# Performance work log

Hardware: AMD Instinct MI355X
Metric: run time of the kernel (lower is better)

## Reference

```python
import jax, jax.numpy as jnp
import numpy as np


def lstm_encode(x, Wih, Whh, b):
    """x: [S, T, F] -> final hidden state [S, H]. PyTorch LSTM gate order (i, f, g, o)."""
    S = x.shape[0]
    H = Whh.shape[1]

    def step(carry, xt):
        h, c = carry
        z = xt @ Wih.T + h @ Whh.T + b  # [S, 4H]
        i, f, g, o = jnp.split(z, 4, axis=-1)
        c = jax.nn.sigmoid(f) * c + jax.nn.sigmoid(i) * jnp.tanh(g)
        h = jax.nn.sigmoid(o) * jnp.tanh(c)
        return (h, c), None

    init = (jnp.zeros((S, H), x.dtype), jnp.zeros((S, H), x.dtype))
    (h, _), _ = jax.lax.scan(step, init, jnp.swapaxes(x, 0, 1))
    return h


def gatv2(h, Ws, Wd, a, bias):
    """Dense GATv2 on batched fully-connected graphs (no self loops).
    h: [G, N, Hin]; Ws, Wd: [nh, Hin, O]; a: [nh, O]; bias: [nh, O] -> [G, N, nh, O].
    Graph is fully connected (all i != j), so edge-softmax == dense row softmax
    with the diagonal masked out; this is the efficient dense form of the
    gather / LeakyReLU / edge-softmax / scatter pattern in DGL's GATv2Conv."""
    nh = Ws.shape[0]
    N = h.shape[1]
    self_mask = jnp.eye(N, dtype=bool)
    outs = []
    for hd in range(nh):  # small fixed head count; loop caps peak memory
        fs = h @ Ws[hd]  # [G, N, O] source-projected feats (messages)
        fd = h @ Wd[hd]  # [G, N, O] dst-projected feats
        e = jax.nn.leaky_relu(fd[:, :, None, :] + fs[:, None, :, :], 0.2)  # [G, dst, src, O]
        logits = jnp.where(self_mask, -jnp.inf, e @ a[hd])  # [G, dst, src]
        attn = jax.nn.softmax(logits, axis=-1)
        outs.append(jnp.einsum('gds,gso->gdo', attn, fs) + bias[hd])
    return jnp.stack(outs, axis=2)


def cosine(x, y, eps=1e-6):
    xn = x / jnp.maximum(jnp.linalg.norm(x, axis=-1, keepdims=True), eps)
    yn = y / jnp.maximum(jnp.linalg.norm(y, axis=-1, keepdims=True), eps)
    return (xn * yn).sum(-1)


def setup_inputs() -> dict:
    key = jax.random.key(0)
    B, K, T, N, F, H, GH, NH = 16, 4, 64, 128, 16, 32, 32, 8
    ks = jax.random.split(key, 16)

    def rn(k, shape, scale=1.0):
        return jax.random.normal(k, shape, jnp.float32) * scale

    return {
        'anchor': rn(ks[0], (B, T, N, F)),
        'pos': rn(ks[1], (B, T, N, F)),
        'neg': rn(ks[2], (B, K, T, N, F)),
        'hideout': rn(ks[3], (B, 2)),
        'timestep': jax.random.uniform(ks[4], (B, 1), jnp.float32),
        'Wih': rn(ks[5], (4 * H, F), 1.0 / np.sqrt(F)),
        'Whh': rn(ks[6], (4 * H, H), 1.0 / np.sqrt(H)),
        'b_lstm': rn(ks[7], (4 * H,), 0.1),
        'W1s': rn(ks[8], (NH, H, H), 1.0 / np.sqrt(H)),
        'W1d': rn(ks[9], (NH, H, H), 1.0 / np.sqrt(H)),
        'a1': rn(ks[10], (NH, H), 1.0 / np.sqrt(H)),
        'b1': rn(ks[11], (NH, H), 0.1),
        'W2s': rn(ks[12], (1, H, GH), 1.0 / np.sqrt(H)),
        'W2d': rn(ks[13], (1, H, GH), 1.0 / np.sqrt(H)),
        'a2': rn(ks[14], (1, GH), 1.0 / np.sqrt(GH)),
        'b2': rn(ks[15], (1, GH), 0.1),
        'num_agents': 128,
    }


def reference(anchor, pos, neg, hideout, timestep, Wih, Whh, b_lstm,
              W1s, W1d, a1, b1, W2s, W2d, a2, b2, num_agents):
    B, T, N, F = anchor.shape
    K = neg.shape[1]
    H = Whh.shape[1]
    # per-agent time series -> LSTM sequences
    a_seq = jnp.transpose(anchor, (0, 2, 1, 3)).reshape(B * N, T, F)
    p_seq = jnp.transpose(pos, (0, 2, 1, 3)).reshape(B * N, T, F)
    n_seq = jnp.transpose(neg, (0, 1, 3, 2, 4)).reshape(B * K * N, T, F)
    hn = lstm_encode(jnp.concatenate([a_seq, p_seq, n_seq], 0), Wih, Whh, b_lstm)
    hg = hn.reshape(-1, N, H)  # [(2+K)*B, N, H] batched fully-connected graphs
    h1 = gatv2(hg, W1s, W1d, a1, b1).mean(axis=2)  # mean over 8 heads
    h2 = gatv2(h1, W2s, W2d, a2, b2)[:, :, 0, :]   # single head, squeezed
    pooled = h2.mean(axis=1)                        # AvgPooling over nodes
    anchor_res = pooled[:B]
    pos_res = pooled[B:2 * B]
    neg_res = pooled[2 * B:].reshape(B, K, -1)
    sim_pos = cosine(anchor_res, pos_res)[:, None]      # [B, 1]
    sim_neg = cosine(anchor_res[:, None, :], neg_res)   # [B, K]
    all_vecs = jnp.concatenate([sim_neg, sim_pos], axis=1)  # positive last
    contrastive = (-jax.nn.log_softmax(all_vecs, axis=1)[:, -1]).mean()
    res = jnp.concatenate([anchor_res, hideout, timestep], axis=-1)
    return res, contrastive
```

## Files before the change

### kernel.cpp

```cpp
#include <hip/hip_runtime.h>
#include <math.h>


typedef __bf16 bf16x8 __attribute__((ext_vector_type(8)));
typedef float  f32x4  __attribute__((ext_vector_type(4)));
typedef unsigned int u32x4 __attribute__((ext_vector_type(4)));

__device__ __forceinline__ float fast_rcp(float x) { return __builtin_amdgcn_rcpf(x); }
__device__ __forceinline__ float sigm(float x)     { return fast_rcp(1.f + __expf(-x)); }
__device__ __forceinline__ float tanh_fast(float x){ return fmaf(2.f, fast_rcp(1.f + __expf(-2.f * x)), -1.f); }

#define KEEP4(x) asm volatile("" : "+v"(x))

#define PAIR_BARRIER() do {                                     \
    asm volatile("s_waitcnt lgkmcnt(0)" ::: "memory");          \
    __builtin_amdgcn_sched_barrier(0);                          \
    __builtin_amdgcn_s_barrier();                               \
    __builtin_amdgcn_sched_barrier(0);                          \
} while (0)

__global__ __launch_bounds__(128, 1) void lstm_mfma_kernel(
    const float* __restrict__ anchor, const float* __restrict__ pos,
    const float* __restrict__ neg, const float* __restrict__ Wih,
    const float* __restrict__ Whh, const float* __restrict__ bias,
    float* __restrict__ hn)
{
    __shared__ unsigned int Hbuf[2][512];
    const int tid  = threadIdx.x;
    const int wid  = tid >> 6;
    const int lane = tid & 63;
    const int l15  = lane & 15;
    const int g4   = lane >> 4;

    #pragma unroll
    for (int i = 0; i < 8; ++i) ((unsigned int*)Hbuf)[tid + i * 128] = 0u;

    u32x4 whhH[4], whhL[4], wihH[4];
    float bq[4];
    #pragma unroll
    for (int G = 0; G < 4; ++G) {
        const int c = G * 32 + wid * 16 + l15;
        bq[G] = bias[c];
        union { u32x4 u; bf16x8 v; } th, tl, ti;
        const float* wr = Whh + c * 32 + g4 * 8;
        #pragma unroll
        for (int i = 0; i < 8; ++i) {
            float wv = wr[i];
            __bf16 hi = (__bf16)wv;
            th.v[i] = hi;
            tl.v[i] = (__bf16)(wv - (float)hi);
        }
        if (g4 < 2) {
            const float* wr2 = Wih + c * 16 + g4 * 8;
            #pragma unroll
            for (int i = 0; i < 8; ++i) ti.v[i] = (__bf16)wr2[i];
        } else {
            #pragma unroll
            for (int i = 0; i < 8; ++i) ti.v[i] = (__bf16)0.f;
        }
        whhH[G] = th.u; whhL[G] = tl.u; wihH[G] = ti.u;
    }
    #pragma unroll
    for (int G = 0; G < 4; ++G) { KEEP4(whhH[G]); KEEP4(whhL[G]); KEEP4(wihH[G]); }

    const int s = blockIdx.x * 16 + l15;
    const float* xbase; int sl;
    if (s < 2048)      { xbase = anchor; sl = s; }
    else if (s < 4096) { xbase = pos;    sl = s - 2048; }
    else               { xbase = neg;    sl = s - 4096; }
    const bool xact = (g4 < 2);
    const float* xp = xbase + (sl >> 7) * 131072 + (sl & 127) * 16 + (xact ? g4 * 8 : 0);

    const float4 z4 = make_float4(0.f, 0.f, 0.f, 0.f);
    float4 xaA = z4, xbA = z4, xaB = z4, xbB = z4;
    if (xact) {
        xaA = *(const float4*)(xp);        xbA = *(const float4*)(xp + 4);
        xaB = *(const float4*)(xp + 2048); xbB = *(const float4*)(xp + 2052);
    }

    float cst[4] = {0,0,0,0};
    float hv[4]  = {0,0,0,0};

    const int c0  = g4 * 2;
    const int swz = (l15 & 3) << 1;
    const int ro0 = l15 * 32 + ((c0 ^ swz) << 2);
    const int ro1 = l15 * 32 + (((c0 + 1) ^ swz) << 2);
    const int jw  = wid * 16 + l15;
    int cur = 0;
    PAIR_BARRIER();

    #define LSTM_STEP(XA, XB)                                                          \
    {                                                                                  \
        const unsigned int* rb = Hbuf[cur];                                            \
        unsigned int*       wb = Hbuf[cur ^ 1];                                        \
        bf16x8 ax;                                                                     \
        ax[0]=(__bf16)XA.x; ax[1]=(__bf16)XA.y; ax[2]=(__bf16)XA.z; ax[3]=(__bf16)XA.w;\
        ax[4]=(__bf16)XB.x; ax[5]=(__bf16)XB.y; ax[6]=(__bf16)XB.z; ax[7]=(__bf16)XB.w;\
        uint4 v0 = *(const uint4*)(rb + ro0);                                          \
        uint4 v1 = *(const uint4*)(rb + ro1);                                          \
        union { unsigned int u[4]; bf16x8 v; } ahi;                                    \
        ahi.u[0] = __builtin_amdgcn_perm(v0.y, v0.x, 0x05040100u);                     \
        ahi.u[1] = __builtin_amdgcn_perm(v0.w, v0.z, 0x05040100u);                     \
        ahi.u[2] = __builtin_amdgcn_perm(v1.y, v1.x, 0x05040100u);                     \
        ahi.u[3] = __builtin_amdgcn_perm(v1.w, v1.z, 0x05040100u);                     \
        f32x4 z[4];                                                                    \
        _Pragma("unroll")                                                              \
        for (int G = 0; G < 4; ++G) {                                                  \
            f32x4 a = __builtin_amdgcn_mfma_f32_16x16x32_bf16(                         \
                ax, __builtin_bit_cast(bf16x8, wihH[G]), (f32x4)(0.f), 0, 0, 0);       \
            a = __builtin_amdgcn_mfma_f32_16x16x32_bf16(                               \
                ahi.v, __builtin_bit_cast(bf16x8, whhH[G]), a, 0, 0, 0);               \
            a = __builtin_amdgcn_mfma_f32_16x16x32_bf16(                               \
                ahi.v, __builtin_bit_cast(bf16x8, whhL[G]), a, 0, 0, 0);               \
            z[G] = a;                                                                  \
        }                                                                              \
        _Pragma("unroll")                                                              \
        for (int r = 0; r < 4; ++r) {                                                  \
            float zi = z[0][r] + bq[0];                                                \
            float zf = z[1][r] + bq[1];                                                \
            float zg = z[2][r] + bq[2];                                                \
            float zo = z[3][r] + bq[3];                                                \
            float cn = fmaf(sigm(zf), cst[r], sigm(zi) * tanh_fast(zg));               \
            cst[r] = cn;                                                               \
            float h = sigm(zo) * tanh_fast(cn);                                        \
            hv[r] = h;                                                                 \
            unsigned int pk = (unsigned int)__builtin_bit_cast(unsigned short,         \
                                                               (__bf16)h);            \
            const int mm = g4 * 4 + r;                                                 \
            wb[mm * 32 + (((jw >> 2) ^ ((mm & 3) << 1)) << 2) + (jw & 3)] = pk;        \
        }                                                                              \
        PAIR_BARRIER();                                                                \
        cur ^= 1;                                                                      \
    }

    for (int t = 0; t < 64; t += 2) {
        float4 cA1 = xaA, cA2 = xbA;
        if (xact && t + 2 < 64) {
            const float* p = xp + (t + 2) * 2048;
            xaA = *(const float4*)(p); xbA = *(const float4*)(p + 4);
        }
        LSTM_STEP(cA1, cA2);

        float4 cB1 = xaB, cB2 = xbB;
        if (xact && t + 3 < 64) {
            const float* p = xp + (t + 3) * 2048;
            xaB = *(const float4*)(p); xbB = *(const float4*)(p + 4);
        }
        LSTM_STEP(cB1, cB2);
    }
    #undef LSTM_STEP

    const int seq0 = blockIdx.x * 16;
    #pragma unroll
    for (int r = 0; r < 4; ++r) {
        hn[(seq0 + g4 * 4 + r) * 32 + jw] = hv[r];
    }
}

__device__ __forceinline__ int fsoff(int n) { return n * 36 + ((n >> 5) << 2); }

__global__ __launch_bounds__(256, 2) void gat1_kernel(
    const float* __restrict__ hn, const float* __restrict__ W1s,
    const float* __restrict__ W1d, const float* __restrict__ a1,
    const float* __restrict__ b1, float* __restrict__ h1heads)
{
    const int g = blockIdx.x >> 3, hd = blockIdx.x & 7;
    __shared__ float FSf[128 * 36 + 16];
    __shared__ float FD[128][36];
    __shared__ float AVr[32];
    __shared__ float As06[128];
    __shared__ float Ad06[128];
    const int tid = threadIdx.x;

    if (tid < 32) AVr[tid] = a1[hd * 32 + tid];

    {
        const int o = tid & 31, nb = tid >> 5;
        float wcs[32], wcd[32];
        const float* wsp = W1s + hd * 1024 + o;
        const float* wdp = W1d + hd * 1024 + o;
        #pragma unroll
        for (int k = 0; k < 32; ++k) { wcs[k] = wsp[k * 32]; wcd[k] = wdp[k * 32]; }
        const float* hp = hn + g * 4096 + nb * 512;
        #pragma unroll 1
        for (int n = 0; n < 16; ++n) {
            const int row = nb * 16 + n;
            float a0 = 0.f, a1_ = 0.f, b0 = 0.f, b1_ = 0.f;
            #pragma unroll
            for (int k0 = 0; k0 < 32; k0 += 4) {
                float4 hv = *(const float4*)(hp + n * 32 + k0);
                a0 = fmaf(hv.x, wcs[k0+0], a0); b0 = fmaf(hv.x, wcd[k0+0], b0);
                a1_ = fmaf(hv.y, wcs[k0+1], a1_); b1_ = fmaf(hv.y, wcd[k0+1], b1_);
                a0 = fmaf(hv.z, wcs[k0+2], a0); b0 = fmaf(hv.z, wcd[k0+2], b0);
                a1_ = fmaf(hv.w, wcs[k0+3], a1_); b1_ = fmaf(hv.w, wcd[k0+3], b1_);
            }
            FSf[fsoff(row) + o] = a0 + a1_;
            FD[row][o] = b0 + b1_;
        }
    }
    __syncthreads();

    if (tid < 128) {
        float ss = 0.f, sd = 0.f;
        const float* fr = FSf + fsoff(tid);
        #pragma unroll
        for (int oo = 0; oo < 32; ++oo) {
            int o = (oo + tid) & 31;
            float a = AVr[o];
            ss = fmaf(a, fr[o], ss);
            sd = fmaf(a, FD[tid][o], sd);
        }
        As06[tid] = 0.6f * ss;
        Ad06[tid] = 0.6f * sd;
    }
    __syncthreads();

    const int p = tid >> 2, sq = tid & 3, sbase = sq << 5;
    const int d0 = p, d1 = p + 64;
    float fdr0[32], fdr1[32], avs[32];
    #pragma unroll
    for (int c = 0; c < 8; ++c) {
        float4 v0 = *(const float4*)&FD[d0][c * 4];
        fdr0[c*4+0] = v0.x; fdr0[c*4+1] = v0.y; fdr0[c*4+2] = v0.z; fdr0[c*4+3] = v0.w;
        float4 v1 = *(const float4*)&FD[d1][c * 4];
        fdr1[c*4+0] = v1.x; fdr1[c*4+1] = v1.y; fdr1[c*4+2] = v1.z; fdr1[c*4+3] = v1.w;
        float4 wv = *(const float4*)&AVr[c * 4];
        avs[c*4+0] = 0.4f * wv.x; avs[c*4+1] = 0.4f * wv.y;
        avs[c*4+2] = 0.4f * wv.z; avs[c*4+3] = 0.4f * wv.w;
    }
    const float adc0 = Ad06[d0], adc1 = Ad06[d1];

    float Z0 = 0.f, Z1 = 0.f;
    float acc0[32], acc1[32];
    #pragma unroll
    for (int o = 0; o < 32; ++o) { acc0[o] = 0.f; acc1[o] = 0.f; }
    #pragma unroll 1
    for (int si = 0; si < 32; ++si) {
        const int s = sbase + si;
        const float* fr = FSf + fsoff(s);
        float4 fa[8];
        #pragma unroll
        for (int c = 0; c < 8; ++c) fa[c] = *(const float4*)(fr + c * 4);
        float c00 = 0.f, c01 = 0.f, c02 = 0.f, c03 = 0.f;
        float c10 = 0.f, c11 = 0.f, c12 = 0.f, c13 = 0.f;
        #pragma unroll
        for (int c = 0; c < 8; ++c) {
            float e;
            e = fdr0[c*4+0] + fa[c].x; c00 = fmaf(avs[c*4+0], __builtin_fabsf(e), c00);
            e = fdr1[c*4+0] + fa[c].x; c10 = fmaf(avs[c*4+0], __builtin_fabsf(e), c10);
            e = fdr0[c*4+1] + fa[c].y; c01 = fmaf(avs[c*4+1], __builtin_fabsf(e), c01);
            e = fdr1[c*4+1] + fa[c].y; c11 = fmaf(avs[c*4+1], __builtin_fabsf(e), c11);
            e = fdr0[c*4+2] + fa[c].z; c02 = fmaf(avs[c*4+2], __builtin_fabsf(e), c02);
            e = fdr1[c*4+2] + fa[c].z; c12 = fmaf(avs[c*4+2], __builtin_fabsf(e), c12);
            e = fdr0[c*4+3] + fa[c].w; c03 = fmaf(avs[c*4+3], __builtin_fabsf(e), c03);
            e = fdr1[c*4+3] + fa[c].w; c13 = fmaf(avs[c*4+3], __builtin_fabsf(e), c13);
        }
        const float ass = As06[s];
        float v0 = adc0 + ass + ((c00 + c01) + (c02 + c03));
        float v1 = adc1 + ass + ((c10 + c11) + (c12 + c13));
        float e0 = (s == d0) ? 0.f : __expf(v0);
        float e1 = (s == d1) ? 0.f : __expf(v1);
        Z0 += e0; Z1 += e1;
        #pragma unroll
        for (int c = 0; c < 8; ++c) {
            acc0[c*4+0] = fmaf(e0, fa[c].x, acc0[c*4+0]);
            acc1[c*4+0] = fmaf(e1, fa[c].x, acc1[c*4+0]);
            acc0[c*4+1] = fmaf(e0, fa[c].y, acc0[c*4+1]);
            acc1[c*4+1] = fmaf(e1, fa[c].y, acc1[c*4+1]);
            acc0[c*4+2] = fmaf(e0, fa[c].z, acc0[c*4+2]);
            acc1[c*4+2] = fmaf(e1, fa[c].z, acc1[c*4+2]);
            acc0[c*4+3] = fmaf(e0, fa[c].w, acc0[c*4+3]);
            acc1[c*4+3] = fmaf(e1, fa[c].w, acc1[c*4+3]);
        }
    }
    Z0 += __shfl_xor(Z0, 1); Z0 += __shfl_xor(Z0, 2);
    Z1 += __shfl_xor(Z1, 1); Z1 += __shfl_xor(Z1, 2);
    const float rz0 = fast_rcp(Z0), rz1 = fast_rcp(Z1);
    #pragma unroll
    for (int o = 0; o < 32; ++o) {
        acc0[o] += __shfl_xor(acc0[o], 1);
        acc0[o] += __shfl_xor(acc0[o], 2);
        acc1[o] += __shfl_xor(acc1[o], 1);
        acc1[o] += __shfl_xor(acc1[o], 2);
    }

    if (sq == 0) {
        const float* bp = b1 + hd * 32;
        float* dst0 = h1heads + ((size_t)((g * 8 + hd) * 128 + d0)) * 32;
        float* dst1 = h1heads + ((size_t)((g * 8 + hd) * 128 + d1)) * 32;
        #pragma unroll
        for (int c = 0; c < 8; ++c) {
            float4 v;
            v.x = fmaf(acc0[c*4+0], rz0, bp[c*4+0]);
            v.y = fmaf(acc0[c*4+1], rz0, bp[c*4+1]);
            v.z = fmaf(acc0[c*4+2], rz0, bp[c*4+2]);
            v.w = fmaf(acc0[c*4+3], rz0, bp[c*4+3]);
            *(float4*)(dst0 + c * 4) = v;
            v.x = fmaf(acc1[c*4+0], rz1, bp[c*4+0]);
            v.y = fmaf(acc1[c*4+1], rz1, bp[c*4+1]);
            v.z = fmaf(acc1[c*4+2], rz1, bp[c*4+2]);
            v.w = fmaf(acc1[c*4+3], rz1, bp[c*4+3]);
            *(float4*)(dst1 + c * 4) = v;
        }
    }
}

__global__ __launch_bounds__(256) void gat2_kernel(
    const float* __restrict__ h1heads, const float* __restrict__ W2s,
    const float* __restrict__ W2d, const float* __restrict__ a2,
    const float* __restrict__ b2, float* __restrict__ pooled)
{
    const int g = blockIdx.x;
    __shared__ float HS[128][36];
    __shared__ float FSf[128 * 36 + 16];
    __shared__ float FD[128][36];
    __shared__ float AVr[32];
    __shared__ float As06[128];
    __shared__ float Ad06[128];
    const int tid = threadIdx.x;

    if (tid < 32) AVr[tid] = a2[tid];

    {
        #pragma unroll
        for (int i = 0; i < 4; ++i) {
            int idx4 = i * 256 + tid;
            float sx = 0.f, sy = 0.f, sz = 0.f, sw = 0.f;
            #pragma unroll
            for (int hdd = 0; hdd < 8; ++hdd) {
                const float4* src = (const float4*)(h1heads + (size_t)(g * 8 + hdd) * 4096);
                float4 v = src[idx4];
                sx += v.x; sy += v.y; sz += v.z; sw += v.w;
            }
            int n = idx4 >> 3, k0 = (idx4 & 7) * 4;
            float4 r; r.x = sx * 0.125f; r.y = sy * 0.125f; r.z = sz * 0.125f; r.w = sw * 0.125f;
            *(float4*)&HS[n][k0] = r;
        }
    }
    __syncthreads();

    {
        const int o = tid & 31, nb = tid >> 5;
        float wcs[32], wcd[32];
        const float* wsp = W2s + o;
        const float* wdp = W2d + o;
        #pragma unroll
        for (int k = 0; k < 32; ++k) { wcs[k] = wsp[k * 32]; wcd[k] = wdp[k * 32]; }
        #pragma unroll 1
        for (int n = nb * 16; n < nb * 16 + 16; ++n) {
            float a0 = 0.f, a1_ = 0.f, b0 = 0.f, b1_ = 0.f;
            #pragma unroll
            for (int k0 = 0; k0 < 32; k0 += 4) {
                const float4 hv = *(const float4*)&HS[n][k0];
                a0 = fmaf(hv.x, wcs[k0+0], a0); b0 = fmaf(hv.x, wcd[k0+0], b0);
                a1_ = fmaf(hv.y, wcs[k0+1], a1_); b1_ = fmaf(hv.y, wcd[k0+1], b1_);
                a0 = fmaf(hv.z, wcs[k0+2], a0); b0 = fmaf(hv.z, wcd[k0+2], b0);
                a1_ = fmaf(hv.w, wcs[k0+3], a1_); b1_ = fmaf(hv.w, wcd[k0+3], b1_);
            }
            FSf[fsoff(n) + o] = a0 + a1_;
            FD[n][o] = b0 + b1_;
        }
    }
    __syncthreads();

    if (tid < 128) {
        float ss = 0.f, sd = 0.f;
        const float* fr = FSf + fsoff(tid);
        #pragma unroll
        for (int oo = 0; oo < 32; ++oo) {
            int o = (oo + tid) & 31;
            float a = AVr[o];
            ss = fmaf(a, fr[o], ss);
            sd = fmaf(a, FD[tid][o], sd);
        }
        As06[tid] = 0.6f * ss;
        Ad06[tid] = 0.6f * sd;
    }
    __syncthreads();

    const int d = tid >> 1, sbase = (tid & 1) << 6;
    float fdr[32], avs[32];
    #pragma unroll
    for (int c = 0; c < 8; ++c) {
        float4 v = *(const float4*)&FD[d][c * 4];
        fdr[c*4+0] = v.x; fdr[c*4+1] = v.y; fdr[c*4+2] = v.z; fdr[c*4+3] = v.w;
        float4 wv = *(const float4*)&AVr[c * 4];
        avs[c*4+0] = 0.4f * wv.x; avs[c*4+1] = 0.4f * wv.y;
        avs[c*4+2] = 0.4f * wv.z; avs[c*4+3] = 0.4f * wv.w;
    }
    const float adc = Ad06[d];

    float Z = 0.f;
    float acc[32];
    #pragma unroll
    for (int o = 0; o < 32; ++o) acc[o] = 0.f;
    #pragma unroll 1
    for (int si = 0; si < 64; ++si) {
        const int s = sbase + si;
        const float* fr = FSf + fsoff(s);
        float4 fa[8];
        #pragma unroll
        for (int c = 0; c < 8; ++c) fa[c] = *(const float4*)(fr + c * 4);
        float c0 = 0.f, c1 = 0.f, c2 = 0.f, c3 = 0.f;
        #pragma unroll
        for (int c = 0; c < 8; ++c) {
            float e0 = fdr[c*4+0] + fa[c].x; c0 = fmaf(avs[c*4+0], __builtin_fabsf(e0), c0);
            float e1 = fdr[c*4+1] + fa[c].y; c1 = fmaf(avs[c*4+1], __builtin_fabsf(e1), c1);
            float e2 = fdr[c*4+2] + fa[c].z; c2 = fmaf(avs[c*4+2], __builtin_fabsf(e2), c2);
            float e3 = fdr[c*4+3] + fa[c].w; c3 = fmaf(avs[c*4+3], __builtin_fabsf(e3), c3);
        }
        float v = adc + As06[s] + ((c0 + c1) + (c2 + c3));
        float e = (s == d) ? 0.f : __expf(v);
        Z += e;
        #pragma unroll
        for (int c = 0; c < 8; ++c) {
            acc[c*4+0] = fmaf(e, fa[c].x, acc[c*4+0]);
            acc[c*4+1] = fmaf(e, fa[c].y, acc[c*4+1]);
            acc[c*4+2] = fmaf(e, fa[c].z, acc[c*4+2]);
            acc[c*4+3] = fmaf(e, fa[c].w, acc[c*4+3]);
        }
    }
    Z += __shfl_xor(Z, 1);
    const float rz = fast_rcp(Z);
    #pragma unroll
    for (int o = 0; o < 32; ++o) acc[o] += __shfl_xor(acc[o], 1);

    __syncthreads();
    if ((tid & 1) == 0) {
        #pragma unroll
        for (int c = 0; c < 4; ++c) {
            float4 v;
            v.x = acc[c*4+0] * rz; v.y = acc[c*4+1] * rz;
            v.z = acc[c*4+2] * rz; v.w = acc[c*4+3] * rz;
            *(float4*)&FD[d][c * 4] = v;
        }
    } else {
        #pragma unroll
        for (int c = 4; c < 8; ++c) {
            float4 v;
            v.x = acc[c*4+0] * rz; v.y = acc[c*4+1] * rz;
            v.z = acc[c*4+2] * rz; v.w = acc[c*4+3] * rz;
            *(float4*)&FD[d][c * 4] = v;
        }
    }
    __syncthreads();

    if (tid < 32) {
        float sp = 0.f;
        #pragma unroll 1
        for (int n = 0; n < 128; ++n) sp += FD[n][tid];
        pooled[g * 32 + tid] = fmaf(sp, 1.f / 128.f, b2[tid]);
    }
}

__global__ void final_kernel(const float* __restrict__ pooled,
                             const float* __restrict__ hideout,
                             const float* __restrict__ timestep,
                             float* __restrict__ out)
{
    const int b = threadIdx.x;
    __shared__ float lossArr[16];
    if (b < 16) {
        const float* A  = pooled + b * 32;
        const float* Pv = pooled + (16 + b) * 32;
        float av[32];
        float na = 0.f;
        #pragma unroll
        for (int i = 0; i < 32; ++i) { av[i] = A[i]; na += av[i] * av[i]; }
        float npv = 0.f, dp = 0.f;
        #pragma unroll
        for (int i = 0; i < 32; ++i) { float p = Pv[i]; npv += p * p; dp += av[i] * p; }
        const float eps = 1e-6f;
        const float ia = 1.f / fmaxf(sqrtf(na), eps);
        const float sp = dp * ia / fmaxf(sqrtf(npv), eps);
        float sn[4];
        #pragma unroll
        for (int k = 0; k < 4; ++k) {
            const float* Nv = pooled + (32 + b * 4 + k) * 32;
            float nn = 0.f, dn = 0.f;
            #pragma unroll
            for (int i = 0; i < 32; ++i) { float q = Nv[i]; nn += q * q; dn += av[i] * q; }
            sn[k] = dn * ia / fmaxf(sqrtf(nn), eps);
        }
        float m = sp;
        #pragma unroll
        for (int k = 0; k < 4; ++k) m = fmaxf(m, sn[k]);
        float Z = expf(sp - m);
        #pragma unroll
        for (int k = 0; k < 4; ++k) Z += expf(sn[k] - m);
        lossArr[b] = logf(Z) + m - sp;
        float* r = out + b * 35;
        #pragma unroll
        for (int i = 0; i < 32; ++i) r[i] = av[i];
        r[32] = hideout[b * 2];
        r[33] = hideout[b * 2 + 1];
        r[34] = timestep[b];
    }
    __syncthreads();
    if (b == 0) {
        float s = 0.f;
        #pragma unroll
        for (int i = 0; i < 16; ++i) s += lossArr[i];
        out[560] = s * (1.f / 16.f);
    }
}

extern "C" void kernel_launch(void* const* d_in, const int* in_sizes, int n_in,
                              void* d_out, int out_size, void* d_ws, size_t ws_size,
                              hipStream_t stream) {
    const float* anchor   = (const float*)d_in[0];
    const float* pos      = (const float*)d_in[1];
    const float* neg      = (const float*)d_in[2];
    const float* hideout  = (const float*)d_in[3];
    const float* timestep = (const float*)d_in[4];
    const float* Wih      = (const float*)d_in[5];
    const float* Whh      = (const float*)d_in[6];
    const float* b_lstm   = (const float*)d_in[7];
    const float* W1s      = (const float*)d_in[8];
    const float* W1d      = (const float*)d_in[9];
    const float* a1       = (const float*)d_in[10];
    const float* b1       = (const float*)d_in[11];
    const float* W2s      = (const float*)d_in[12];
    const float* W2d      = (const float*)d_in[13];
    const float* a2       = (const float*)d_in[14];
    const float* b2       = (const float*)d_in[15];
    float* out = (float*)d_out;

    char* ws = (char*)d_ws;
    float* hn      = (float*)(ws);
    float* h1heads = (float*)(ws + 1605632);
    float* pooled  = (float*)(ws + 14188544);

    hipLaunchKernelGGL(lstm_mfma_kernel, dim3(768), dim3(128), 0, stream,
                       anchor, pos, neg, Wih, Whh, b_lstm, hn);
    hipLaunchKernelGGL(gat1_kernel,  dim3(768),  dim3(256), 0, stream,
                       hn, W1s, W1d, a1, b1, h1heads);
    hipLaunchKernelGGL(gat2_kernel,  dim3(96),   dim3(256), 0, stream,
                       h1heads, W2s, W2d, a2, b2, pooled);
    hipLaunchKernelGGL(final_kernel, dim3(1),    dim3(64),  0, stream,
                       pooled, hideout, timestep, out);
}
```

Measured before the change: 175.2 us.

## Split LSTM gates across eight waves with LDS exchange of preactivations

The LSTM block grows from 2 to 8 waves, so each wave now computes the MFMA for a single gate/half pair instead of all four gates. Gate preactivations are written to a shared-memory buffer, and after a barrier each thread reads the four gates for one (sequence, hidden) element to apply the nonlinearities. This shortens each wave's serial MFMA and activation chain per timestep. In exchange it adds a second block-wide barrier per step, extra LDS traffic, and a larger workgroup that may lower the number of resident blocks per CU.

```diff
diff --git a/kernel.cpp b/kernel.cpp
--- a/kernel.cpp
+++ b/kernel.cpp
@@ -12,35 +12,29 @@
 
 #define KEEP4(x) asm volatile("" : "+v"(x))
 
-#define PAIR_BARRIER() do {                                     \
-    asm volatile("s_waitcnt lgkmcnt(0)" ::: "memory");          \
-    __builtin_amdgcn_sched_barrier(0);                          \
-    __builtin_amdgcn_s_barrier();                               \
-    __builtin_amdgcn_sched_barrier(0);                          \
-} while (0)
-
-__global__ __launch_bounds__(128, 1) void lstm_mfma_kernel(
+__global__ __launch_bounds__(512, 1) void lstm_mfma_kernel(
     const float* __restrict__ anchor, const float* __restrict__ pos,
     const float* __restrict__ neg, const float* __restrict__ Wih,
     const float* __restrict__ Whh, const float* __restrict__ bias,
     float* __restrict__ hn)
 {
+    __shared__ float Zl[8 * 320];
     __shared__ unsigned int Hbuf[2][512];
     const int tid  = threadIdx.x;
-    const int wid  = tid >> 6;
+    const int w    = tid >> 6;
     const int lane = tid & 63;
     const int l15  = lane & 15;
     const int g4   = lane >> 4;
-
-    #pragma unroll
-    for (int i = 0; i < 8; ++i) ((unsigned int*)Hbuf)[tid + i * 128] = 0u;
-
-    u32x4 whhH[4], whhL[4], wihH[4];
-    float bq[4];
-    #pragma unroll
-    for (int G = 0; G < 4; ++G) {
-        const int c = G * 32 + wid * 16 + l15;
-        bq[G] = bias[c];
+    const int am   = tid >> 5;
+    const int aj   = tid & 31;
+
+    #pragma unroll
+    for (int i = 0; i < 2; ++i) ((unsigned int*)Hbuf)[tid + i * 512] = 0u;
+
+    const int G = w >> 1, Hh = w & 1;
+    const int c = G * 32 + Hh * 16 + l15;
+    u32x4 whhH, whhL, wihH;
+    {
         union { u32x4 u; bf16x8 v; } th, tl, ti;
         const float* wr = Whh + c * 32 + g4 * 8;
         #pragma unroll
@@ -58,10 +52,11 @@
             #pragma unroll
             for (int i = 0; i < 8; ++i) ti.v[i] = (__bf16)0.f;
         }
-        whhH[G] = th.u; whhL[G] = tl.u; wihH[G] = ti.u;
-    }
-    #pragma unroll
-    for (int G = 0; G < 4; ++G) { KEEP4(whhH[G]); KEEP4(whhL[G]); KEEP4(wihH[G]); }
+        whhH = th.u; whhL = tl.u; wihH = ti.u;
+    }
+    KEEP4(whhH); KEEP4(whhL); KEEP4(wihH);
+
+    const float bi = bias[aj], bf_ = bias[32 + aj], bg = bias[64 + aj], bo = bias[96 + aj];
 
     const int s = blockIdx.x * 16 + l15;
     const float* xbase; int sl;
@@ -78,58 +73,52 @@
         xaB = *(const float4*)(xp + 2048); xbB = *(const float4*)(xp + 2052);
     }
 
-    float cst[4] = {0,0,0,0};
-    float hv[4]  = {0,0,0,0};
+    float cstA = 0.f, hA = 0.f;
 
     const int c0  = g4 * 2;
     const int swz = (l15 & 3) << 1;
     const int ro0 = l15 * 32 + ((c0 ^ swz) << 2);
     const int ro1 = l15 * 32 + (((c0 + 1) ^ swz) << 2);
-    const int jw  = wid * 16 + l15;
+    const int zw  = w * 320 + l15 * 20 + g4 * 4;
+    const int tHh = aj >> 4, jc = (aj & 15) * 20 + am;
+    const int zr_i = (0 | tHh) * 320 + jc;
+    const int zr_f = (2 | tHh) * 320 + jc;
+    const int zr_g = (4 | tHh) * 320 + jc;
+    const int zr_o = (6 | tHh) * 320 + jc;
+    const int hw   = am * 32 + (((aj >> 2) ^ ((am & 3) << 1)) << 2) + (aj & 3);
     int cur = 0;
-    PAIR_BARRIER();
+    __syncthreads();
 
     #define LSTM_STEP(XA, XB)                                                          \
     {                                                                                  \
-        const unsigned int* rb = Hbuf[cur];                                            \
-        unsigned int*       wb = Hbuf[cur ^ 1];                                        \
         bf16x8 ax;                                                                     \
         ax[0]=(__bf16)XA.x; ax[1]=(__bf16)XA.y; ax[2]=(__bf16)XA.z; ax[3]=(__bf16)XA.w;\
         ax[4]=(__bf16)XB.x; ax[5]=(__bf16)XB.y; ax[6]=(__bf16)XB.z; ax[7]=(__bf16)XB.w;\
-        uint4 v0 = *(const uint4*)(rb + ro0);                                          \
-        uint4 v1 = *(const uint4*)(rb + ro1);                                          \
+        uint4 v0 = *(const uint4*)(Hbuf[cur] + ro0);                                   \
+        uint4 v1 = *(const uint4*)(Hbuf[cur] + ro1);                                   \
         union { unsigned int u[4]; bf16x8 v; } ahi;                                    \
         ahi.u[0] = __builtin_amdgcn_perm(v0.y, v0.x, 0x05040100u);                     \
         ahi.u[1] = __builtin_amdgcn_perm(v0.w, v0.z, 0x05040100u);                     \
         ahi.u[2] = __builtin_amdgcn_perm(v1.y, v1.x, 0x05040100u);                     \
         ahi.u[3] = __builtin_amdgcn_perm(v1.w, v1.z, 0x05040100u);                     \
-        f32x4 z[4];                                                                    \
-        _Pragma("unroll")                                                              \
-        for (int G = 0; G < 4; ++G) {                                                  \
-            f32x4 a = __builtin_amdgcn_mfma_f32_16x16x32_bf16(                         \
-                ax, __builtin_bit_cast(bf16x8, wihH[G]), (f32x4)(0.f), 0, 0, 0);       \
-            a = __builtin_amdgcn_mfma_f32_16x16x32_bf16(                               \
-                ahi.v, __builtin_bit_cast(bf16x8, whhH[G]), a, 0, 0, 0);               \
-            a = __builtin_amdgcn_mfma_f32_16x16x32_bf16(                               \
-                ahi.v, __builtin_bit_cast(bf16x8, whhL[G]), a, 0, 0, 0);               \
-            z[G] = a;                                                                  \
-        }                                                                              \
-        _Pragma("unroll")                                                              \
-        for (int r = 0; r < 4; ++r) {                                                  \
-            float zi = z[0][r] + bq[0];                                                \
-            float zf = z[1][r] + bq[1];                                                \
-            float zg = z[2][r] + bq[2];                                                \
-            float zo = z[3][r] + bq[3];                                                \
-            float cn = fmaf(sigm(zf), cst[r], sigm(zi) * tanh_fast(zg));               \
-            cst[r] = cn;                                                               \
-            float h = sigm(zo) * tanh_fast(cn);                                        \
-            hv[r] = h;                                                                 \
-            unsigned int pk = (unsigned int)__builtin_bit_cast(unsigned short,         \
-                                                               (__bf16)h);            \
-            const int mm = g4 * 4 + r;                                                 \
-            wb[mm * 32 + (((jw >> 2) ^ ((mm & 3) << 1)) << 2) + (jw & 3)] = pk;        \
-        }                                                                              \
-        PAIR_BARRIER();                                                                \
+        f32x4 a = __builtin_amdgcn_mfma_f32_16x16x32_bf16(                             \
+            ax, __builtin_bit_cast(bf16x8, wihH), (f32x4)(0.f), 0, 0, 0);              \
+        a = __builtin_amdgcn_mfma_f32_16x16x32_bf16(                                   \
+            ahi.v, __builtin_bit_cast(bf16x8, whhH), a, 0, 0, 0);                      \
+        a = __builtin_amdgcn_mfma_f32_16x16x32_bf16(                                   \
+            ahi.v, __builtin_bit_cast(bf16x8, whhL), a, 0, 0, 0);                      \
+        *(f32x4*)(Zl + zw) = a;                                                        \
+        __syncthreads();                                                               \
+        float zi = Zl[zr_i] + bi;                                                      \
+        float zf = Zl[zr_f] + bf_;                                                     \
+        float zg = Zl[zr_g] + bg;                                                      \
+        float zo = Zl[zr_o] + bo;                                                      \
+        float cn = fmaf(sigm(zf), cstA, sigm(zi) * tanh_fast(zg));                     \
+        cstA = cn;                                                                     \
+        hA = sigm(zo) * tanh_fast(cn);                                                 \
+        Hbuf[cur ^ 1][hw] = (unsigned int)__builtin_bit_cast(unsigned short,           \
+                                                             (__bf16)hA);             \
+        __syncthreads();                                                               \
         cur ^= 1;                                                                      \
     }
 
@@ -150,11 +139,7 @@
     }
     #undef LSTM_STEP
 
-    const int seq0 = blockIdx.x * 16;
-    #pragma unroll
-    for (int r = 0; r < 4; ++r) {
-        hn[(seq0 + g4 * 4 + r) * 32 + jw] = hv[r];
-    }
+    hn[(blockIdx.x * 16 + am) * 32 + aj] = hA;
 }
 
 __device__ __forceinline__ int fsoff(int n) { return n * 36 + ((n >> 5) << 2); }
@@ -531,7 +516,7 @@
     float* h1heads = (float*)(ws + 1605632);
     float* pooled  = (float*)(ws + 14188544);
 
-    hipLaunchKernelGGL(lstm_mfma_kernel, dim3(768), dim3(128), 0, stream,
+    hipLaunchKernelGGL(lstm_mfma_kernel, dim3(768), dim3(512), 0, stream,
                        anchor, pos, neg, Wih, Whh, b_lstm, hn);
     hipLaunchKernelGGL(gat1_kernel,  dim3(768),  dim3(256), 0, stream,
                        hn, W1s, W1d, a1, b1, h1heads);
```

Result: faster. 159.2 us (-9.1%).
